# Optimization experiments

Hardware: AMD Instinct MI355X
Metric: run time of the kernel (lower is better)

## Reference

```python
import jax, jax.numpy as jnp
import numpy as np

K = 3
K2 = K * K
G = 8  # groups = out_channels // K^2 = 72 // 9


def conv2d(x, w, b, padding, dilation):
    out = jax.lax.conv_general_dilated(
        x, w, window_strides=(1, 1),
        padding=[(padding[0], padding[0]), (padding[1], padding[1])],
        rhs_dilation=dilation,
        dimension_numbers=('NCHW', 'OIHW', 'NCHW'))
    return out + b[None, :, None, None]


def deform_agg(x, offset, dynw, stride=1, padding=1, dilation=1):
    """DCNv4-style modulated deformable aggregation.
    x: [B,C,H,W]; offset: [B,2,K2,Ho,Wo] (dy,dx per kernel point);
    dynw: [B,G*K2,Ho,Wo] dynamic per-location aggregation weights.
    out[b,c,h,w] = sum_k dynw[b,g(c)*K2+k,h,w] * bilinear(x[b,c], p_k(h,w)+off_k).
    """
    B, C, H, W = x.shape
    Ho, Wo = dynw.shape[2], dynw.shape[3]
    Cg = C // G
    ii = jnp.arange(K2) // K
    jj = jnp.arange(K2) % K
    base_y = (jnp.arange(Ho)[None, :, None] * stride - padding + ii[:, None, None] * dilation)  # [K2,Ho,1]
    base_x = (jnp.arange(Wo)[None, None, :] * stride - padding + jj[:, None, None] * dilation)  # [K2,1,Wo]
    py = base_y[None].astype(x.dtype) + offset[:, 0]  # [B,K2,Ho,Wo]
    px = base_x[None].astype(x.dtype) + offset[:, 1]
    y0f = jnp.floor(py)
    x0f = jnp.floor(px)
    fy = py - y0f
    fx = px - x0f
    y0 = y0f.astype(jnp.int32)
    x0 = x0f.astype(jnp.int32)
    bidx = jnp.arange(B)[:, None, None, None]

    def gather(yi, xi):
        valid = (yi >= 0) & (yi < H) & (xi >= 0) & (xi < W)
        v = x[bidx, :, jnp.clip(yi, 0, H - 1), jnp.clip(xi, 0, W - 1)]  # [B,K2,Ho,Wo,C]
        return v * valid[..., None].astype(x.dtype)

    w00 = ((1 - fy) * (1 - fx))[..., None]
    w01 = ((1 - fy) * fx)[..., None]
    w10 = (fy * (1 - fx))[..., None]
    w11 = (fy * fx)[..., None]
    val = (gather(y0, x0) * w00 + gather(y0, x0 + 1) * w01
           + gather(y0 + 1, x0) * w10 + gather(y0 + 1, x0 + 1) * w11)  # [B,K2,Ho,Wo,C]

    dynw_r = dynw.reshape(B, G, K2, Ho, Wo)
    val_r = val.reshape(B, K2, Ho, Wo, G, Cg)
    out = jnp.einsum('bgkhw,bkhwgc->bgchw', dynw_r, val_r)
    return out.reshape(B, C, Ho, Wo)


def setup_inputs() -> dict:
    key = jax.random.key(0)
    ks = jax.random.split(key, 9)
    B, C, H, W = 2, 128, 160, 160
    OC = G * K2  # 72
    std_h = 1.0 / np.sqrt(C * K)  # fan-in of (1,K) conv
    std_v = 1.0 / np.sqrt(C * K)  # fan-in of (K,1) conv
    return {
        'x': jax.random.normal(ks[0], (B, C, H, W), jnp.float32),
        'w_hoff': jax.random.normal(ks[1], (2 * K2, C, 1, K), jnp.float32) * std_h,
        'b_hoff': jnp.zeros((2 * K2,), jnp.float32),
        'w_hw': jax.random.normal(ks[2], (OC, C, 1, K), jnp.float32) * std_h,
        'b_hw': jnp.zeros((OC,), jnp.float32),
        'w_voff': jax.random.normal(ks[3], (2 * K2, C, K, 1), jnp.float32) * std_v,
        'b_voff': jnp.zeros((2 * K2,), jnp.float32),
        'w_vw': jax.random.normal(ks[4], (OC, C, K, 1), jnp.float32) * std_v,
        'b_vw': jnp.zeros((OC,), jnp.float32),
    }


def reference(x, w_hoff, b_hoff, w_hw, b_hw, w_voff, b_voff, w_vw, b_vw):
    B, C, H, W = x.shape
    # horizontal branch: (1,K) convs for offsets + dynamic weights
    off_h = conv2d(x, w_hoff, b_hoff, (0, 1), (1, 1)).reshape(B, 2, K2, H, W)
    dyn_h = conv2d(x, w_hw, b_hw, (0, 1), (1, 1))
    # vertical branch: (K,1) convs (both computed from x, as in the source)
    off_v = conv2d(x, w_voff, b_voff, (1, 0), (1, 1)).reshape(B, 2, K2, H, W)
    dyn_v = conv2d(x, w_vw, b_vw, (1, 0), (1, 1))
    out_h = deform_agg(x, off_h, dyn_h, stride=1, padding=1, dilation=1)
    out_v = deform_agg(out_h, off_v, dyn_v, stride=1, padding=1, dilation=1)
    return out_v
```

## Files before the change

### kernel.cpp

```cpp
#include <hip/hip_runtime.h>
#include <hip/hip_bf16.h>
#include <cmath>

constexpr int Cch = 128;
constexpr int Hc = 160;
constexpr int Wc = 160;
constexpr int HWc = Hc * Wc;
constexpr int NPIX = 2 * HWc;

typedef __attribute__((ext_vector_type(8))) short bf16x8;
typedef __attribute__((ext_vector_type(4))) float f32x4;

static __device__ __forceinline__ short f2bf(float v) {
    __hip_bfloat16 h = __float2bfloat16(v);
    return *reinterpret_cast<short*>(&h);
}
static __device__ __forceinline__ float bf2f(short s) {
    __hip_bfloat16 h = *reinterpret_cast<__hip_bfloat16*>(&s);
    return __bfloat162float(h);
}

__global__ void wprep2_k(const float* __restrict__ wh_off, const float* __restrict__ wh_dyn,
                         const float* __restrict__ wv_off, const float* __restrict__ wv_dyn,
                         const float* __restrict__ bh_off, const float* __restrict__ bh_dyn,
                         const float* __restrict__ bv_off, const float* __restrict__ bv_dyn,
                         short* __restrict__ whi, short* __restrict__ wlo,
                         float* __restrict__ bias) {
    int idx = blockIdx.x * 256 + threadIdx.x;
    int j = idx & 7;
    int oc = (idx >> 3) & 31;
    int t = idx >> 8;
    int kb = t % 48;
    int grp = t / 48;
    int third = grp % 3, dir = grp / 3;
    int tap = kb >> 4, ks = (kb >> 2) & 3, kgrp = kb & 3;
    int ocg = third * 32 + oc;
    int c = ks * 32 + kgrp * 8 + j;
    const float* woff = dir ? wv_off : wh_off;
    const float* wdyn = dir ? wv_dyn : wh_dyn;
    float v = 0.f;
    if (ocg < 18) v = woff[(ocg * Cch + c) * 3 + tap];
    else if (ocg < 90) v = wdyn[((ocg - 18) * Cch + c) * 3 + tap];
    short hi = f2bf(v);
    whi[idx] = hi;
    wlo[idx] = f2bf(v - bf2f(hi));
    if (idx < 192) {
        int d2 = idx / 96, jb = idx % 96;
        const float* boff = d2 ? bv_off : bh_off;
        const float* bdyn = d2 ? bv_dyn : bh_dyn;
        bias[idx] = jb < 18 ? boff[jb] : (jb < 90 ? bdyn[jb - 18] : 0.f);
    }
}

__global__ void pack_k(const float* __restrict__ x, float* __restrict__ xT,
                       short* __restrict__ xh, short* __restrict__ xl) {
    __shared__ float tile[32][33];
    int b = blockIdx.z;
    int j0 = blockIdx.x * 32;
    int i0 = blockIdx.y * 32;
    const float* inb = x + (size_t)b * Cch * HWc;
    for (int di = threadIdx.y; di < 32; di += 8)
        tile[di][threadIdx.x] = inb[(size_t)(i0 + di) * HWc + j0 + threadIdx.x];
    __syncthreads();
    size_t obase = (size_t)b * HWc * Cch;
    for (int dj = threadIdx.y; dj < 32; dj += 8) {
        int hw = j0 + dj, c = i0 + threadIdx.x;
        float v = tile[threadIdx.x][dj];
        size_t o = obase + (size_t)hw * Cch + c;
        xT[o] = v;
        short hi = f2bf(v);
        xh[o] = hi;
        xl[o] = f2bf(v - bf2f(hi));
    }
}

__global__ __launch_bounds__(256) void conv_mfma_k(
        const short* __restrict__ xh, const short* __restrict__ xl,
        const short* __restrict__ whi, const short* __restrict__ wlo,
        const float* __restrict__ bias,
        float* __restrict__ convH, float* __restrict__ convV) {
    __shared__ short sh_h[12288];
    __shared__ short sh_l[12288];
    int grpi = blockIdx.x;
    int dir = grpi / 3, third = grpi - dir * 3;
    int tid = threadIdx.x;
    int lane = tid & 63;
    int wid = tid >> 6;
    int l15 = lane & 15;
    int kgrp = lane >> 4;

    {
        const bf16x8* srcH = reinterpret_cast<const bf16x8*>(whi + (size_t)grpi * 12288);
        const bf16x8* srcL = reinterpret_cast<const bf16x8*>(wlo + (size_t)grpi * 12288);
        bf16x8* dstH = reinterpret_cast<bf16x8*>(sh_h);
        bf16x8* dstL = reinterpret_cast<bf16x8*>(sh_l);
#pragma unroll
        for (int i = 0; i < 6; ++i) {
            dstH[tid + i * 256] = srcH[tid + i * 256];
            dstL[tid + i * 256] = srcL[tid + i * 256];
        }
    }
    __syncthreads();

    int px0 = blockIdx.y * 128 + wid * 32;

    int pxA = px0 + l15;
    int pxB = px0 + 16 + l15;
    int bA = pxA >= HWc, bB = pxB >= HWc;
    int hwA = pxA - bA * HWc, hwB = pxB - bB * HWc;
    int hA = hwA / Wc, wA = hwA - hA * Wc;
    int hB = hwB / Wc, wB = hwB - hB * Wc;

    f32x4 acc[2][2];
#pragma unroll
    for (int m = 0; m < 2; ++m)
#pragma unroll
        for (int n = 0; n < 2; ++n) acc[m][n] = f32x4{0.f, 0.f, 0.f, 0.f};

#pragma unroll
    for (int tap = 0; tap < 3; ++tap) {
        int d = tap - 1;
        int vcA, vcB, shwA, shwB;
        if (dir == 0) { vcA = wA + d; shwA = hwA + d; vcB = wB + d; shwB = hwB + d; }
        else          { vcA = hA + d; shwA = hwA + d * Wc; vcB = hB + d; shwB = hwB + d * Wc; }
        bool valA = (unsigned)vcA < 160u;
        bool valB = (unsigned)vcB < 160u;
        int rA = bA * HWc + min(max(shwA, 0), HWc - 1);
        int rB = bB * HWc + min(max(shwB, 0), HWc - 1);
        const short* apA_h = xh + (size_t)rA * Cch + kgrp * 8;
        const short* apA_l = xl + (size_t)rA * Cch + kgrp * 8;
        const short* apB_h = xh + (size_t)rB * Cch + kgrp * 8;
        const short* apB_l = xl + (size_t)rB * Cch + kgrp * 8;
#pragma unroll
        for (int ks = 0; ks < 4; ++ks) {
            bf16x8 ah0 = *reinterpret_cast<const bf16x8*>(apA_h + ks * 32);
            bf16x8 al0 = *reinterpret_cast<const bf16x8*>(apA_l + ks * 32);
            bf16x8 ah1 = *reinterpret_cast<const bf16x8*>(apB_h + ks * 32);
            bf16x8 al1 = *reinterpret_cast<const bf16x8*>(apB_l + ks * 32);
            if (!valA) { ah0 = bf16x8{}; al0 = bf16x8{}; }
            if (!valB) { ah1 = bf16x8{}; al1 = bf16x8{}; }
            int kb = tap * 16 + ks * 4 + kgrp;
            const short* bp = &sh_h[(kb * 32 + l15) * 8];
            const short* bq = &sh_l[(kb * 32 + l15) * 8];
            bf16x8 bh0 = *reinterpret_cast<const bf16x8*>(bp);
            bf16x8 bh1 = *reinterpret_cast<const bf16x8*>(bp + 128);
            bf16x8 bl0 = *reinterpret_cast<const bf16x8*>(bq);
            bf16x8 bl1 = *reinterpret_cast<const bf16x8*>(bq + 128);
            acc[0][0] = __builtin_amdgcn_mfma_f32_16x16x32_bf16(ah0, bh0, acc[0][0], 0, 0, 0);
            acc[0][1] = __builtin_amdgcn_mfma_f32_16x16x32_bf16(ah0, bh1, acc[0][1], 0, 0, 0);
            acc[1][0] = __builtin_amdgcn_mfma_f32_16x16x32_bf16(ah1, bh0, acc[1][0], 0, 0, 0);
            acc[1][1] = __builtin_amdgcn_mfma_f32_16x16x32_bf16(ah1, bh1, acc[1][1], 0, 0, 0);
            acc[0][0] = __builtin_amdgcn_mfma_f32_16x16x32_bf16(al0, bh0, acc[0][0], 0, 0, 0);
            acc[0][1] = __builtin_amdgcn_mfma_f32_16x16x32_bf16(al0, bh1, acc[0][1], 0, 0, 0);
            acc[1][0] = __builtin_amdgcn_mfma_f32_16x16x32_bf16(al1, bh0, acc[1][0], 0, 0, 0);
            acc[1][1] = __builtin_amdgcn_mfma_f32_16x16x32_bf16(al1, bh1, acc[1][1], 0, 0, 0);
            acc[0][0] = __builtin_amdgcn_mfma_f32_16x16x32_bf16(ah0, bl0, acc[0][0], 0, 0, 0);
            acc[0][1] = __builtin_amdgcn_mfma_f32_16x16x32_bf16(ah0, bl1, acc[0][1], 0, 0, 0);
            acc[1][0] = __builtin_amdgcn_mfma_f32_16x16x32_bf16(ah1, bl0, acc[1][0], 0, 0, 0);
            acc[1][1] = __builtin_amdgcn_mfma_f32_16x16x32_bf16(ah1, bl1, acc[1][1], 0, 0, 0);
        }
    }

    float* outp = dir ? convV : convH;
#pragma unroll
    for (int n = 0; n < 2; ++n) {
        int col = third * 32 + n * 16 + l15;
        float bv = bias[dir * 96 + col];
#pragma unroll
        for (int m = 0; m < 2; ++m) {
#pragma unroll
            for (int r = 0; r < 4; ++r) {
                int prow = px0 + m * 16 + kgrp * 4 + r;
                outp[(size_t)prow * 96 + col] = acc[m][n][r] + bv;
            }
        }
    }
}

__global__ __launch_bounds__(256) void deform_k(const float* __restrict__ xT,
                                                const float* __restrict__ cv,
                                                float* __restrict__ outT) {
    int tid = threadIdx.x;
    int lane = tid & 63;
    int half = lane >> 5;
    int cl = (lane & 31) * 4;
    int pix = blockIdx.x * 8 + (tid >> 6) * 2 + half;
    int b = pix >= HWc;
    int hw = pix - b * HWc;
    int h = hw / Wc;
    int w = hw - h * Wc;
    int g = (lane & 31) >> 2;

    const float* cp = cv + (size_t)pix * 96;
    const float* xb = xT + (size_t)b * HWc * Cch;

    float4 acc = make_float4(0.f, 0.f, 0.f, 0.f);
#pragma unroll
    for (int k = 0; k < 9; ++k) {
        float dy = cp[k];
        float dx = cp[9 + k];
        float wt = cp[18 + g * 9 + k];
        float py = (float)(h - 1 + k / 3) + dy;
        float px = (float)(w - 1 + k % 3) + dx;
        float y0f = floorf(py), x0f = floorf(px);
        float fy = py - y0f, fx = px - x0f;
        int y0 = (int)y0f, x0 = (int)x0f;
        int y1 = y0 + 1, x1 = x0 + 1;
        float w00 = (1.f - fy) * (1.f - fx) * wt;
        float w01 = (1.f - fy) * fx * wt;
        float w10 = fy * (1.f - fx) * wt;
        float w11 = fy * fx * wt;

        {
            bool v = (y0 >= 0) & (y0 < Hc) & (x0 >= 0) & (x0 < Wc);
            int yc = min(max(y0, 0), Hc - 1), xc = min(max(x0, 0), Wc - 1);
            float4 t = *reinterpret_cast<const float4*>(&xb[((size_t)yc * Wc + xc) * Cch + cl]);
            float m = v ? w00 : 0.f;
            acc.x = fmaf(m, t.x, acc.x); acc.y = fmaf(m, t.y, acc.y);
            acc.z = fmaf(m, t.z, acc.z); acc.w = fmaf(m, t.w, acc.w);
        }
        {
            bool v = (y0 >= 0) & (y0 < Hc) & (x1 >= 0) & (x1 < Wc);
            int yc = min(max(y0, 0), Hc - 1), xc = min(max(x1, 0), Wc - 1);
            float4 t = *reinterpret_cast<const float4*>(&xb[((size_t)yc * Wc + xc) * Cch + cl]);
            float m = v ? w01 : 0.f;
            acc.x = fmaf(m, t.x, acc.x); acc.y = fmaf(m, t.y, acc.y);
            acc.z = fmaf(m, t.z, acc.z); acc.w = fmaf(m, t.w, acc.w);
        }
        {
            bool v = (y1 >= 0) & (y1 < Hc) & (x0 >= 0) & (x0 < Wc);
            int yc = min(max(y1, 0), Hc - 1), xc = min(max(x0, 0), Wc - 1);
            float4 t = *reinterpret_cast<const float4*>(&xb[((size_t)yc * Wc + xc) * Cch + cl]);
            float m = v ? w10 : 0.f;
            acc.x = fmaf(m, t.x, acc.x); acc.y = fmaf(m, t.y, acc.y);
            acc.z = fmaf(m, t.z, acc.z); acc.w = fmaf(m, t.w, acc.w);
        }
        {
            bool v = (y1 >= 0) & (y1 < Hc) & (x1 >= 0) & (x1 < Wc);
            int yc = min(max(y1, 0), Hc - 1), xc = min(max(x1, 0), Wc - 1);
            float4 t = *reinterpret_cast<const float4*>(&xb[((size_t)yc * Wc + xc) * Cch + cl]);
            float m = v ? w11 : 0.f;
            acc.x = fmaf(m, t.x, acc.x); acc.y = fmaf(m, t.y, acc.y);
            acc.z = fmaf(m, t.z, acc.z); acc.w = fmaf(m, t.w, acc.w);
        }
    }
    *reinterpret_cast<float4*>(&outT[(size_t)pix * Cch + cl]) = acc;
}

__global__ void transpose_k(const float* __restrict__ in, float* __restrict__ out,
                            int R, int Cn) {
    __shared__ float tile[32][33];
    int b = blockIdx.z;
    const float* inb = in + (size_t)b * R * Cn;
    float* outb = out + (size_t)b * R * Cn;
    int j0 = blockIdx.x * 32;
    int i0 = blockIdx.y * 32;
    for (int di = threadIdx.y; di < 32; di += 8) {
        int i = i0 + di, j = j0 + threadIdx.x;
        if (i < R && j < Cn) tile[di][threadIdx.x] = inb[(size_t)i * Cn + j];
    }
    __syncthreads();
    for (int dj = threadIdx.y; dj < 32; dj += 8) {
        int j = j0 + dj, i = i0 + threadIdx.x;
        if (j < Cn && i < R) outb[(size_t)j * R + i] = tile[threadIdx.x][dj];
    }
}

extern "C" void kernel_launch(void* const* d_in, const int* in_sizes, int n_in,
                              void* d_out, int out_size, void* d_ws, size_t ws_size,
                              hipStream_t stream) {
    const float* x      = (const float*)d_in[0];
    const float* w_hoff = (const float*)d_in[1];
    const float* b_hoff = (const float*)d_in[2];
    const float* w_hw   = (const float*)d_in[3];
    const float* b_hw   = (const float*)d_in[4];
    const float* w_voff = (const float*)d_in[5];
    const float* b_voff = (const float*)d_in[6];
    const float* w_vw   = (const float*)d_in[7];
    const float* b_vw   = (const float*)d_in[8];
    float* out = (float*)d_out;
    char* ws = (char*)d_ws;

    short* whi  = (short*)(ws + 0);
    short* wlo  = (short*)(ws + 147456);
    float* bias = (float*)(ws + 294912);
    float* xT   = (float*)(ws + 295680);
    short* xh   = (short*)(ws + 26510080);
    short* xl   = (short*)(ws + 39617280);
    float* convH = (float*)(ws + 52724480);
    float* convV = (float*)(ws + 72385280);
    float* outh = (float*)xh;
    float* outv = xT;

    hipLaunchKernelGGL(wprep2_k, dim3(288), dim3(256), 0, stream,
                       w_hoff, w_hw, w_voff, w_vw, b_hoff, b_hw, b_voff, b_vw,
                       whi, wlo, bias);

    hipLaunchKernelGGL(pack_k, dim3(800, 4, 2), dim3(32, 8), 0, stream,
                       x, xT, xh, xl);

    hipLaunchKernelGGL(conv_mfma_k, dim3(6, 400), dim3(256), 0, stream,
                       xh, xl, whi, wlo, bias, convH, convV);

    hipLaunchKernelGGL(deform_k, dim3(6400), dim3(256), 0, stream,
                       xT, convH, outh);
    hipLaunchKernelGGL(deform_k, dim3(6400), dim3(256), 0, stream,
                       outh, convV, outv);

    hipLaunchKernelGGL(transpose_k, dim3(4, 800, 2), dim3(32, 8), 0, stream,
                       outv, out, 25600, 128);
}
```

Baseline: 262.1 us.

## Enlarge conv MFMA pixel tile and remap block order for XCD locality

The conv kernel now gives each wave 64 pixels instead of 32, so four M-subtiles reuse each set of LDS weight fragments. This halves the weight staging per pixel and uses a 1D grid of 1200 blocks. Both the conv and deform kernels remap blockIdx so that contiguous work chunks land on the same XCD (blockIdx & 7), which should improve L2 locality for neighbouring pixel reads. The trade-offs are higher register pressure from 8 accumulators plus 8 A fragments, and fewer blocks, which may lower occupancy.

```diff
diff --git a/kernel.cpp b/kernel.cpp
--- a/kernel.cpp
+++ b/kernel.cpp
@@ -81,7 +81,9 @@
         float* __restrict__ convH, float* __restrict__ convV) {
     __shared__ short sh_h[12288];
     __shared__ short sh_l[12288];
-    int grpi = blockIdx.x;
+    int work = (blockIdx.x & 7) * 150 + (blockIdx.x >> 3);
+    int ytile = work / 6;
+    int grpi = work - ytile * 6;
     int dir = grpi / 3, third = grpi - dir * 3;
     int tid = threadIdx.x;
     int lane = tid & 63;
@@ -102,43 +104,48 @@
     }
     __syncthreads();
 
-    int px0 = blockIdx.y * 128 + wid * 32;
-
-    int pxA = px0 + l15;
-    int pxB = px0 + 16 + l15;
-    int bA = pxA >= HWc, bB = pxB >= HWc;
-    int hwA = pxA - bA * HWc, hwB = pxB - bB * HWc;
-    int hA = hwA / Wc, wA = hwA - hA * Wc;
-    int hB = hwB / Wc, wB = hwB - hB * Wc;
-
-    f32x4 acc[2][2];
-#pragma unroll
-    for (int m = 0; m < 2; ++m)
+    int px0 = ytile * 256 + wid * 64;
+
+    int bm[4], hwm[4], hm[4], wm[4];
+#pragma unroll
+    for (int m = 0; m < 4; ++m) {
+        int px = px0 + m * 16 + l15;
+        int bb = px >= HWc;
+        int hw = px - bb * HWc;
+        bm[m] = bb; hwm[m] = hw;
+        hm[m] = hw / Wc; wm[m] = hw - hm[m] * Wc;
+    }
+
+    f32x4 acc[4][2];
+#pragma unroll
+    for (int m = 0; m < 4; ++m)
 #pragma unroll
         for (int n = 0; n < 2; ++n) acc[m][n] = f32x4{0.f, 0.f, 0.f, 0.f};
 
 #pragma unroll
     for (int tap = 0; tap < 3; ++tap) {
         int d = tap - 1;
-        int vcA, vcB, shwA, shwB;
-        if (dir == 0) { vcA = wA + d; shwA = hwA + d; vcB = wB + d; shwB = hwB + d; }
-        else          { vcA = hA + d; shwA = hwA + d * Wc; vcB = hB + d; shwB = hwB + d * Wc; }
-        bool valA = (unsigned)vcA < 160u;
-        bool valB = (unsigned)vcB < 160u;
-        int rA = bA * HWc + min(max(shwA, 0), HWc - 1);
-        int rB = bB * HWc + min(max(shwB, 0), HWc - 1);
-        const short* apA_h = xh + (size_t)rA * Cch + kgrp * 8;
-        const short* apA_l = xl + (size_t)rA * Cch + kgrp * 8;
-        const short* apB_h = xh + (size_t)rB * Cch + kgrp * 8;
-        const short* apB_l = xl + (size_t)rB * Cch + kgrp * 8;
+        const short* aph[4];
+        const short* apl[4];
+        bool val[4];
+#pragma unroll
+        for (int m = 0; m < 4; ++m) {
+            int vc = (dir == 0) ? (wm[m] + d) : (hm[m] + d);
+            int shw = hwm[m] + ((dir == 0) ? d : d * Wc);
+            val[m] = (unsigned)vc < 160u;
+            int r = bm[m] * HWc + min(max(shw, 0), HWc - 1);
+            aph[m] = xh + (size_t)r * Cch + kgrp * 8;
+            apl[m] = xl + (size_t)r * Cch + kgrp * 8;
+        }
 #pragma unroll
         for (int ks = 0; ks < 4; ++ks) {
-            bf16x8 ah0 = *reinterpret_cast<const bf16x8*>(apA_h + ks * 32);
-            bf16x8 al0 = *reinterpret_cast<const bf16x8*>(apA_l + ks * 32);
-            bf16x8 ah1 = *reinterpret_cast<const bf16x8*>(apB_h + ks * 32);
-            bf16x8 al1 = *reinterpret_cast<const bf16x8*>(apB_l + ks * 32);
-            if (!valA) { ah0 = bf16x8{}; al0 = bf16x8{}; }
-            if (!valB) { ah1 = bf16x8{}; al1 = bf16x8{}; }
+            bf16x8 ah[4], al[4];
+#pragma unroll
+            for (int m = 0; m < 4; ++m) {
+                ah[m] = *reinterpret_cast<const bf16x8*>(aph[m] + ks * 32);
+                al[m] = *reinterpret_cast<const bf16x8*>(apl[m] + ks * 32);
+                if (!val[m]) { ah[m] = bf16x8{}; al[m] = bf16x8{}; }
+            }
             int kb = tap * 16 + ks * 4 + kgrp;
             const short* bp = &sh_h[(kb * 32 + l15) * 8];
             const short* bq = &sh_l[(kb * 32 + l15) * 8];
@@ -146,18 +153,21 @@
             bf16x8 bh1 = *reinterpret_cast<const bf16x8*>(bp + 128);
             bf16x8 bl0 = *reinterpret_cast<const bf16x8*>(bq);
             bf16x8 bl1 = *reinterpret_cast<const bf16x8*>(bq + 128);
-            acc[0][0] = __builtin_amdgcn_mfma_f32_16x16x32_bf16(ah0, bh0, acc[0][0], 0, 0, 0);
-            acc[0][1] = __builtin_amdgcn_mfma_f32_16x16x32_bf16(ah0, bh1, acc[0][1], 0, 0, 0);
-            acc[1][0] = __builtin_amdgcn_mfma_f32_16x16x32_bf16(ah1, bh0, acc[1][0], 0, 0, 0);
-            acc[1][1] = __builtin_amdgcn_mfma_f32_16x16x32_bf16(ah1, bh1, acc[1][1], 0, 0, 0);
-            acc[0][0] = __builtin_amdgcn_mfma_f32_16x16x32_bf16(al0, bh0, acc[0][0], 0, 0, 0);
-            acc[0][1] = __builtin_amdgcn_mfma_f32_16x16x32_bf16(al0, bh1, acc[0][1], 0, 0, 0);
-            acc[1][0] = __builtin_amdgcn_mfma_f32_16x16x32_bf16(al1, bh0, acc[1][0], 0, 0, 0);
-            acc[1][1] = __builtin_amdgcn_mfma_f32_16x16x32_bf16(al1, bh1, acc[1][1], 0, 0, 0);
-            acc[0][0] = __builtin_amdgcn_mfma_f32_16x16x32_bf16(ah0, bl0, acc[0][0], 0, 0, 0);
-            acc[0][1] = __builtin_amdgcn_mfma_f32_16x16x32_bf16(ah0, bl1, acc[0][1], 0, 0, 0);
-            acc[1][0] = __builtin_amdgcn_mfma_f32_16x16x32_bf16(ah1, bl0, acc[1][0], 0, 0, 0);
-            acc[1][1] = __builtin_amdgcn_mfma_f32_16x16x32_bf16(ah1, bl1, acc[1][1], 0, 0, 0);
+#pragma unroll
+            for (int m = 0; m < 4; ++m) {
+                acc[m][0] = __builtin_amdgcn_mfma_f32_16x16x32_bf16(ah[m], bh0, acc[m][0], 0, 0, 0);
+                acc[m][1] = __builtin_amdgcn_mfma_f32_16x16x32_bf16(ah[m], bh1, acc[m][1], 0, 0, 0);
+            }
+#pragma unroll
+            for (int m = 0; m < 4; ++m) {
+                acc[m][0] = __builtin_amdgcn_mfma_f32_16x16x32_bf16(al[m], bh0, acc[m][0], 0, 0, 0);
+                acc[m][1] = __builtin_amdgcn_mfma_f32_16x16x32_bf16(al[m], bh1, acc[m][1], 0, 0, 0);
+            }
+#pragma unroll
+            for (int m = 0; m < 4; ++m) {
+                acc[m][0] = __builtin_amdgcn_mfma_f32_16x16x32_bf16(ah[m], bl0, acc[m][0], 0, 0, 0);
+                acc[m][1] = __builtin_amdgcn_mfma_f32_16x16x32_bf16(ah[m], bl1, acc[m][1], 0, 0, 0);
+            }
         }
     }
 
@@ -167,7 +177,7 @@
         int col = third * 32 + n * 16 + l15;
         float bv = bias[dir * 96 + col];
 #pragma unroll
-        for (int m = 0; m < 2; ++m) {
+        for (int m = 0; m < 4; ++m) {
 #pragma unroll
             for (int r = 0; r < 4; ++r) {
                 int prow = px0 + m * 16 + kgrp * 4 + r;
@@ -184,7 +194,8 @@
     int lane = tid & 63;
     int half = lane >> 5;
     int cl = (lane & 31) * 4;
-    int pix = blockIdx.x * 8 + (tid >> 6) * 2 + half;
+    int work = (blockIdx.x & 7) * 800 + (blockIdx.x >> 3);
+    int pix = work * 8 + (tid >> 6) * 2 + half;
     int b = pix >= HWc;
     int hw = pix - b * HWc;
     int h = hw / Wc;
@@ -299,7 +310,7 @@
     hipLaunchKernelGGL(pack_k, dim3(800, 4, 2), dim3(32, 8), 0, stream,
                        x, xT, xh, xl);
 
-    hipLaunchKernelGGL(conv_mfma_k, dim3(6, 400), dim3(256), 0, stream,
+    hipLaunchKernelGGL(conv_mfma_k, dim3(1200), dim3(256), 0, stream,
                        xh, xl, whi, wlo, bias, convH, convV);
 
     hipLaunchKernelGGL(deform_k, dim3(6400), dim3(256), 0, stream,
```

After: 242.7 us. -7.4%, faster.
